# Kernel tuning notes

Measured on AMD Instinct MI355X. Metric: run time of the kernel, lower is better.

Reference implementation:

```python
import jax, jax.numpy as jnp
import numpy as np

P = 6            # number of polynomial moment potentials phi_j(x) = x^j, j=1..P
SIGMA = 0.5      # diffusion coefficient
REG = (1e-3, 0.0, 0.0)  # (scale, threshold, bump) diagonal regularization of G
N_SAMPLES = 2_000_000
N_TIME = 33


def _moments(x):
    # x: (N,1) -> (N,P) with phi_j(x) = x^j (exponents are integral floats, pow is exact)
    js = jnp.arange(1, P + 1, dtype=x.dtype)
    return x ** js


def _grad_pot(x):
    # grad phi_j(x) = j * x^(j-1): (N,1) -> (N,P)
    js = jnp.arange(1, P + 1, dtype=x.dtype)
    return js * x ** (js - 1)


def _G(x):
    # Gram matrix of potential gradients, (P,P), with diagonal regularization
    g = _grad_pot(x)                      # (N,P)
    G = g.T @ g / x.shape[0]
    d = jnp.diag(G)
    d = jnp.where(d < REG[1], d + REG[2], d)
    return G + REG[0] * jnp.diag(d)


def _interp(x_0, x_1, tk):
    # 'Cos' stochastic interpolant I_t = cos(pi t/2) x_0 + sin(pi t/2) x_1
    a = jnp.cos(jnp.pi * tk / 2)
    b = jnp.sin(jnp.pi * tk / 2)
    return a * x_0 + b * x_1


def _dinterp(x_0, x_1, tk):
    c = jnp.pi / 2
    return c * (-jnp.sin(jnp.pi * tk / 2) * x_0 + jnp.cos(jnp.pi * tk / 2) * x_1)


def _rhs_dt(I, Idot):
    # mean_n grad_phi(I)_np * Idot_n  -> (P,)
    return jnp.einsum('np,n->p', _grad_pot(I), Idot[:, 0]) / I.shape[0]


def _sde_forward(x_1, x_0, x_k, t):
    K = t.shape[0]
    key = jax.random.key(42)

    @jax.checkpoint
    def step(x, k):
        tk = t[k]
        tk1 = t[k + 1]
        h = tk1 - tk
        # predictor: eta_k solves G(x_k) eta = E[grad phi(I_k) . dI_k/dt]
        I_k = _interp(x_0, x_1, tk)
        Idot_k = _dinterp(x_0, x_1, tk)
        eta = jnp.linalg.solve(_G(x), _rhs_dt(I_k, Idot_k))       # (P,)
        drift = _grad_pot(x) @ eta                                 # (N,)
        noise = jnp.sqrt(2 * h) * SIGMA * jax.random.normal(
            jax.random.fold_in(key, k), x.shape, x.dtype)
        y = x + h * drift[:, None] + noise
        # corrector: theta_k matches moments of y to the interpolant at t_{k+1}
        I_k1 = _interp(x_0, x_1, tk1)
        bpe = _moments(I_k1).mean(0)                               # (P,)
        rhs_cc = bpe - _moments(y).mean(0)
        theta = jnp.linalg.solve(_G(y), rhs_cc)                    # (P,)
        x_next = y + (_grad_pot(y) @ theta)[:, None]
        theta = theta / (h * SIGMA ** 2)
        dtphi = _rhs_dt(I_k1, Idot_k)   # source uses gradient_interpolant(k) here
        dH = -theta @ dtphi
        bpp = _moments(x_next).mean(0)
        return x_next, (eta, theta, dH, bpe, bpp)

    x_final, (etas, thetas, dHs, bpe_s, bpp_s) = jax.lax.scan(step, x_k, jnp.arange(K - 1))
    # torch code appends the last stored quantities once more after the loop
    barphi_e = jnp.concatenate([_moments(x_0).mean(0)[None], bpe_s, bpe_s[-1:]], 0)
    barphi_p = jnp.concatenate([_moments(x_k).mean(0)[None], bpp_s, bpp_s[-1:]], 0)
    eta_all = jnp.concatenate([etas, etas[-1:]], 0)
    theta_all = jnp.concatenate([thetas, thetas[-1:]], 0)
    dH_all = jnp.concatenate([dHs, dHs[-1:]], 0)
    return x_final, barphi_e, barphi_p, eta_all, theta_all, dH_all


def setup_inputs() -> dict:
    key = jax.random.key(0)
    k1, k2, k3 = jax.random.split(key, 3)
    return {
        'x_1': jax.random.normal(k1, (N_SAMPLES, 1), jnp.float32),
        'x_0': jax.random.normal(k2, (N_SAMPLES, 1), jnp.float32),
        'x_k': jax.random.normal(k3, (N_SAMPLES, 1), jnp.float32),
        't': jnp.linspace(0.0, 1.0, N_TIME, dtype=jnp.float32),
    }


def reference(x_1, x_0, x_k, t):
    return _sde_forward(x_1, x_0, x_k, t)
```

## Files before the change

kernel.cpp:

```cpp
#include <hip/hip_runtime.h>
#include <stdint.h>

#define N_SAMP  2000000
#define NF4     500000
#define NSTEP   32
#define INV_N   (1.0/2000000.0)
#define NBUCK   64
#define GRID    512
#define NWORK   511
#define BLKSZ   256

#define OUT_BE  2000000
#define OUT_BP  2000204
#define OUT_ETA 2000408
#define OUT_TH  2000606
#define OUT_DH  2000804

#define O_JB    0
#define O_SYB   (37*NBUCK)
#define O_SXB   (O_SYB + NSTEP*10*NBUCK)
#define O_END   (O_SXB + NSTEP*10*NBUCK)
#define WS_BYTES (O_END*8 + 1152*4)

#define CFENCE() __atomic_signal_fence(__ATOMIC_SEQ_CST)
#define WAITVM() __builtin_amdgcn_s_waitcnt(0)

__device__ inline uint32_t uld(const uint32_t* p) {
  return __hip_atomic_load(p, __ATOMIC_RELAXED, __HIP_MEMORY_SCOPE_AGENT);
}
__device__ inline void ust(uint32_t* p, uint32_t v) {
  __hip_atomic_store(p, v, __ATOMIC_RELAXED, __HIP_MEMORY_SCOPE_AGENT);
}
__device__ inline void uadd(uint32_t* p, uint32_t v) {
  __hip_atomic_fetch_add(p, v, __ATOMIC_RELAXED, __HIP_MEMORY_SCOPE_AGENT);
}
__device__ inline double dld(const double* p) {
  return __hip_atomic_load(p, __ATOMIC_RELAXED, __HIP_MEMORY_SCOPE_AGENT);
}
__device__ inline float fld(const float* p) {
  return __hip_atomic_load(p, __ATOMIC_RELAXED, __HIP_MEMORY_SCOPE_AGENT);
}
__device__ inline void fst(float* p, float v) {
  __hip_atomic_store(p, v, __ATOMIC_RELAXED, __HIP_MEMORY_SCOPE_AGENT);
}

__host__ __device__ inline void threefry2x32(uint32_t k0, uint32_t k1,
                                             uint32_t c0, uint32_t c1,
                                             uint32_t* o0, uint32_t* o1) {
  uint32_t ks2 = k0 ^ k1 ^ 0x1BD11BDAu;
  uint32_t x0 = c0 + k0;
  uint32_t x1 = c1 + k1;
#define TF_ROT(x, d) (((x) << (d)) | ((x) >> (32 - (d))))
#define TF_R(a,b,c,d, ka, kb, inc) \
  x0 += x1; x1 = TF_ROT(x1, a); x1 ^= x0; \
  x0 += x1; x1 = TF_ROT(x1, b); x1 ^= x0; \
  x0 += x1; x1 = TF_ROT(x1, c); x1 ^= x0; \
  x0 += x1; x1 = TF_ROT(x1, d); x1 ^= x0; \
  x0 += (ka); x1 += (kb) + (inc);
  TF_R(13,15,26,6,  k1,  ks2, 1u)
  TF_R(17,29,16,24, ks2, k0,  2u)
  TF_R(13,15,26,6,  k0,  k1,  3u)
  TF_R(17,29,16,24, k1,  ks2, 4u)
  TF_R(13,15,26,6,  ks2, k0,  5u)
#undef TF_R
#undef TF_ROT
  *o0 = x0; *o1 = x1;
}

__device__ inline float bits_to_normal(uint32_t bits) {
  float f = __uint_as_float((bits >> 9) | 0x3f800000u) - 1.0f;
  const float lo = -0.99999994f;
  float u = f * 2.0f + lo;
  u = fmaxf(lo, u);
  float w = -log1pf(-u * u);
  float p;
  if (w < 5.0f) {
    w = w - 2.5f;
    p = 2.81022636e-08f;
    p = fmaf(p, w, 3.43273939e-07f);
    p = fmaf(p, w, -3.5233877e-06f);
    p = fmaf(p, w, -4.39150654e-06f);
    p = fmaf(p, w, 0.00021858087f);
    p = fmaf(p, w, -0.00125372503f);
    p = fmaf(p, w, -0.00417768164f);
    p = fmaf(p, w, 0.246640727f);
    p = fmaf(p, w, 1.50140941f);
  } else {
    w = sqrtf(w) - 3.0f;
    p = -0.000200214257f;
    p = fmaf(p, w, 0.000100950558f);
    p = fmaf(p, w, 0.00134934322f);
    p = fmaf(p, w, -0.00367342844f);
    p = fmaf(p, w, 0.00573950773f);
    p = fmaf(p, w, -0.0076224613f);
    p = fmaf(p, w, 0.00943887047f);
    p = fmaf(p, w, 1.00167406f);
    p = fmaf(p, w, 2.83297682f);
  }
  return __uint_as_float(0x3FB504F3u) * (p * u);
}

__device__ inline double wave_gauss6(const double S[11], double rv, int lane) {
  int r = (lane < 6) ? lane : 0;
  double row[6];
#pragma unroll
  for (int j = 0; j < 6; j++) row[j] = (double)((r + 1) * (j + 1)) * S[r + j];
  row[r] *= 1.001;
#pragma unroll
  for (int c = 0; c < 6; c++) {
    double pr[6], prh;
#pragma unroll
    for (int j = 0; j < 6; j++) pr[j] = __shfl(row[j], c, 64);
    prh = __shfl(rv, c, 64);
    if (lane > c && lane < 6) {
      double f = row[c] / pr[c];
#pragma unroll
      for (int j = 0; j < 6; j++) row[j] -= f * pr[j];
      rv -= f * prh;
    }
  }
  double xv = 0.0;
#pragma unroll
  for (int rr = 5; rr >= 0; rr--) {
    double cand = rv / row[rr];
    double xr = __shfl(cand, rr, 64);
    if (lane == rr) xv = xr;
    if (lane < rr) rv -= row[rr] * xr;
  }
  return xv;
}

__device__ inline void wait_leaves(const uint32_t* leaf, uint32_t target, int lane) {
  for (;;) {
    uint32_t v = uld(&leaf[lane & 31]);
#pragma unroll
    for (int off = 16; off; off >>= 1) v += __shfl_xor(v, off, 64);
    if (v >= target) break;
    __builtin_amdgcn_s_sleep(2);
  }
  CFENCE();
}

__device__ inline void get_S(const double* B, int lane, double S[11]) {
  S[0] = 1.0;
#pragma unroll
  for (int q = 0; q < 10; q++) {
    double s = dld(&B[q * NBUCK + lane]);
#pragma unroll
    for (int off = 32; off; off >>= 1) s += __shfl_xor(s, off, 64);
    S[q + 1] = s * INV_N;
  }
}

template <int NQ>
__device__ inline void block_bucket(float acc[NQ], double* __restrict__ buck,
                                    float smf[4][37], int lane, int wid, int t,
                                    int bidx) {
#pragma unroll
  for (int q = 0; q < NQ; q++) {
    float v = acc[q];
#pragma unroll
    for (int off = 32; off; off >>= 1) v += __shfl_down(v, off, 64);
    if (lane == 0) smf[wid][q] = v;
  }
  __syncthreads();
  if (t < NQ) {
    double s = (double)smf[0][t] + (double)smf[1][t] +
               (double)smf[2][t] + (double)smf[3][t];
    atomicAdd(&buck[t * NBUCK + bidx], s);
  }
}

__global__ __launch_bounds__(BLKSZ, 2) void k_all(
    const float* __restrict__ x1g, const float* __restrict__ x0g,
    const float* __restrict__ xkg, const float* __restrict__ tg,
    float* __restrict__ out, double* __restrict__ WD, uint32_t* __restrict__ WU) {
  __shared__ float smf[4][37];
  __shared__ float sC[8];
  __shared__ double sMsc[37];
  __shared__ float sF[NSTEP * 20];
  __shared__ uint32_t sK[NSTEP][2];

  const int t = threadIdx.x;
  const int lane = t & 63, wid = t >> 6;
  double* JB  = WD + O_JB;
  double* SYB = WD + O_SYB;
  double* SXB = WD + O_SXB;
  float* COEFP = (float*)WU;
  float* COEFC = (float*)(WU + 8);
  uint32_t* leaf0 = WU + 32;
  uint32_t* leafP = WU + 64;
  uint32_t* leafC = WU + 96;
  uint32_t* seqP  = WU + 128;
  uint32_t* seqC  = WU + 640;

  if (blockIdx.x == 0) {
    if (t >= 64) return;
    wait_leaves(leaf0, NWORK, lane);
    for (int q = 0; q < 37; q++) {
      double s = dld(&JB[q * NBUCK + lane]);
#pragma unroll
      for (int off = 32; off; off >>= 1) s += __shfl_xor(s, off, 64);
      if (lane == 0) sMsc[q] = s * INV_N;
    }
#define MG(A, B_) (((A) == 0 && (B_) == 0) ? 1.0 : \
    sMsc[(((A) + (B_) + 2) * ((A) + (B_) - 1)) / 2 + (A)])
    if (lane < NSTEP) {
      const double Bd[7][7] = {
          {1,0,0,0,0,0,0},{1,1,0,0,0,0,0},{1,2,1,0,0,0,0},{1,3,3,1,0,0,0},
          {1,4,6,4,1,0,0},{1,5,10,10,5,1,0},{1,6,15,20,15,6,1}};
      int k = lane;
      float tk = tg[k], tk1 = tg[k + 1];
      float h = tk1 - tk;
      float ns = sqrtf(2.0f * h) * 0.5f;
      const float PI_F = 3.14159274f;
      double a  = (double)cosf((PI_F * tk) * 0.5f);
      double b  = (double)sinf((PI_F * tk) * 0.5f);
      double a1 = (double)cosf((PI_F * tk1) * 0.5f);
      double b1 = (double)sinf((PI_F * tk1) * 0.5f);
      const double C2 = (double)1.57079637f;
      double pa[7], pb[7], pa1[7], pb1[7];
      pa[0] = pb[0] = pa1[0] = pb1[0] = 1.0;
      for (int i = 1; i < 7; i++) {
        pa[i] = pa[i-1] * a;   pb[i] = pb[i-1] * b;
        pa1[i] = pa1[i-1] * a1; pb1[i] = pb1[i-1] * b1;
      }
      sF[k * 20 + 0] = h;
      sF[k * 20 + 1] = ns;
      for (int p = 1; p <= 6; p++) {
        double s_rhs = 0, s_bpe = 0, s_dt = 0;
        for (int j = 0; j < p; j++) {
          double term = -b * MG(j + 1, p - 1 - j) + a * MG(j, p - j);
          s_rhs += Bd[p-1][j] * pa[j]  * pb[p-1-j]  * term;
          s_dt  += Bd[p-1][j] * pa1[j] * pb1[p-1-j] * term;
        }
        for (int j = 0; j <= p; j++)
          s_bpe += Bd[p][j] * pa1[j] * pb1[p - j] * MG(j, p - j);
        float fr = (float)((double)p * C2 * s_rhs);
        float be = (float)s_bpe;
        sF[k * 20 + 2 + p - 1]  = fr;
        sF[k * 20 + 8 + p - 1]  = be;
        sF[k * 20 + 14 + p - 1] = (float)((double)p * C2 * s_dt);
        out[OUT_BE + (k + 1) * 6 + (p - 1)] = be;
        if (k == NSTEP - 1) out[OUT_BE + (NSTEP + 1) * 6 + (p - 1)] = be;
      }
    }
    if (lane < 6) {
      int p = lane + 1;
      out[OUT_BE + lane] = (float)MG(p, 0);
      out[OUT_BP + lane] = (float)sMsc[27 + lane];
    }
#undef MG
    {
      double S[11];
      S[0] = 1.0;
#pragma unroll
      for (int q = 0; q < 10; q++) S[q + 1] = sMsc[27 + q];
      double rv = (lane < 6) ? (double)sF[2 + lane] : 0.0;
      double xv = wave_gauss6(S, rv, lane);
      if (lane < 6) {
        out[OUT_ETA + lane] = (float)xv;
        fst(&COEFP[lane], (float)xv * (float)(lane + 1));
      }
      if (lane == 6) fst(&COEFP[6], sF[0]);
      if (lane == 7) fst(&COEFP[7], sF[1]);
      CFENCE(); WAITVM();
      if (lane < 32) ust(&seqP[lane * 16], 1u);
    }
    for (int k = 0; k < NSTEP; k++) {
      wait_leaves(leafP, (uint32_t)(NWORK * (k + 1)), lane);
      {
        double S[11];
        get_S(SYB + k * 10 * NBUCK, lane, S);
        double rv = (lane < 6) ? ((double)sF[k*20 + 8 + lane] - S[lane + 1]) : 0.0;
        double xv = wave_gauss6(S, rv, lane);
        if (lane < 6) fst(&COEFC[lane], (float)xv * (float)(lane + 1));
        float h = sF[k * 20];
        float th = (float)xv / (h * 0.25f);
        if (lane < 6) {
          out[OUT_TH + k * 6 + lane] = th;
          if (k == NSTEP - 1) out[OUT_TH + NSTEP * 6 + lane] = th;
        }
        float contrib = (lane < 6) ? th * sF[k*20 + 14 + lane] : 0.f;
#pragma unroll
        for (int off = 4; off; off >>= 1) contrib += __shfl_down(contrib, off, 64);
        if (lane == 0) {
          float dH = -contrib;
          out[OUT_DH + k] = dH;
          if (k == NSTEP - 1) out[OUT_DH + NSTEP] = dH;
        }
        CFENCE(); WAITVM();
        if (lane < 32) ust(&seqC[lane * 16], (uint32_t)(k + 1));
      }
      wait_leaves(leafC, (uint32_t)(NWORK * (k + 1)), lane);
      {
        double S[11];
        get_S(SXB + k * 10 * NBUCK, lane, S);
        if (lane < 6) {
          float bp = (float)S[lane + 1];
          out[OUT_BP + (k + 1) * 6 + lane] = bp;
          if (k == NSTEP - 1) out[OUT_BP + (NSTEP + 1) * 6 + lane] = bp;
        }
        if (k < NSTEP - 1) {
          double rv = (lane < 6) ? (double)sF[(k+1)*20 + 2 + lane] : 0.0;
          double xv = wave_gauss6(S, rv, lane);
          if (lane < 6) {
            float v = (float)xv;
            out[OUT_ETA + (k + 1) * 6 + lane] = v;
            if (k + 1 == NSTEP - 1) out[OUT_ETA + NSTEP * 6 + lane] = v;
            fst(&COEFP[lane], v * (float)(lane + 1));
          }
          if (lane == 6) fst(&COEFP[6], sF[(k+1) * 20 + 0]);
          if (lane == 7) fst(&COEFP[7], sF[(k+1) * 20 + 1]);
          CFENCE(); WAITVM();
          if (lane < 32) ust(&seqP[lane * 16], (uint32_t)(k + 2));
        }
      }
    }
    return;
  }

  const int wb = blockIdx.x - 1;
  const int bidx = blockIdx.x & (NBUCK - 1);
  const int myseq = (blockIdx.x & 31) * 16;
  int f4[4]; bool vld[4];
  float st[16];
  float nz[16];
  if (t < NSTEP) threefry2x32(0u, 42u, 0u, (uint32_t)t, &sK[t][0], &sK[t][1]);
#pragma unroll
  for (int c = 0; c < 4; c++) { f4[c] = (wb * 4 + c) * 256 + t; vld[c] = f4[c] < NF4; }

  {
    float a37[37];
#pragma unroll
    for (int q = 0; q < 37; q++) a37[q] = 0.f;
#pragma unroll
    for (int c = 0; c < 4; c++) {
      if (vld[c]) {
        float4 xk4 = ((const float4*)xkg)[f4[c]];
        float4 x04 = ((const float4*)x0g)[f4[c]];
        float4 x14 = ((const float4*)x1g)[f4[c]];
        float xk_[4] = {xk4.x, xk4.y, xk4.z, xk4.w};
        float x0_[4] = {x04.x, x04.y, x04.z, x04.w};
        float x1_[4] = {x14.x, x14.y, x14.z, x14.w};
#pragma unroll
        for (int r = 0; r < 4; r++) {
          st[c * 4 + r] = xk_[r];
          float p0[7], p1[7];
          p0[0] = 1.f; p1[0] = 1.f;
#pragma unroll
          for (int m = 0; m < 6; m++) { p0[m+1] = p0[m]*x0_[r]; p1[m+1] = p1[m]*x1_[r]; }
          int q = 0;
#pragma unroll
          for (int s = 1; s <= 6; s++)
#pragma unroll
            for (int a = 0; a <= s; a++) a37[q++] += p0[a] * p1[s - a];
          float xp = xk_[r];
          a37[27] += xp;
#pragma unroll
          for (int m = 1; m < 10; m++) { xp *= xk_[r]; a37[27 + m] += xp; }
        }
      } else {
#pragma unroll
        for (int r = 0; r < 4; r++) st[c * 4 + r] = 0.f;
      }
    }
    block_bucket<37>(a37, JB, smf, lane, wid, t, bidx);
    if (t == 0) { CFENCE(); WAITVM(); uadd(&leaf0[blockIdx.x & 31], 1u); }
  }

#pragma unroll
  for (int c = 0; c < 4; c++) {
    if (vld[c]) {
      uint32_t base = (uint32_t)(f4[c] * 4);
#pragma unroll
      for (int r = 0; r < 4; r++) {
        uint32_t o0, o1;
        threefry2x32(sK[0][0], sK[0][1], 0u, base + (uint32_t)r, &o0, &o1);
        nz[c * 4 + r] = bits_to_normal(o0 ^ o1);
      }
    }
  }

  for (int k = 0; k < NSTEP; k++) {
    if (t == 0) {
      while (uld(&seqP[myseq]) < (uint32_t)(k + 1)) __builtin_amdgcn_s_sleep(2);
      CFENCE();
#pragma unroll
      for (int i = 0; i < 8; i++) sC[i] = fld(&COEFP[i]);
    }
    __syncthreads();
    {
      float c0 = sC[0], c1 = sC[1], c2 = sC[2], c3 = sC[3];
      float c4 = sC[4], c5 = sC[5], h = sC[6], ns = sC[7];
      float acc[10];
#pragma unroll
      for (int q = 0; q < 10; q++) acc[q] = 0.f;
#pragma unroll
      for (int c = 0; c < 4; c++) {
        if (vld[c]) {
#pragma unroll
          for (int r = 0; r < 4; r++) {
            float x = st[c * 4 + r];
            float d = c0 + x*(c1 + x*(c2 + x*(c3 + x*(c4 + x*c5))));
            float y = x + h * d + ns * nz[c * 4 + r];
            st[c * 4 + r] = y;
            float pw = y;
            acc[0] += pw;
#pragma unroll
            for (int m = 1; m < 10; m++) { pw *= y; acc[m] += pw; }
          }
        }
      }
      block_bucket<10>(acc, SYB + k * 10 * NBUCK, smf, lane, wid, t, bidx);
      if (t == 0) { CFENCE(); WAITVM(); uadd(&leafP[blockIdx.x & 31], 1u); }
    }
    if (k + 1 < NSTEP) {
      uint32_t ka = sK[k + 1][0], kb = sK[k + 1][1];
#pragma unroll
      for (int c = 0; c < 4; c++) {
        if (vld[c]) {
          uint32_t base = (uint32_t)(f4[c] * 4);
#pragma unroll
          for (int r = 0; r < 4; r++) {
            uint32_t o0, o1;
            threefry2x32(ka, kb, 0u, base + (uint32_t)r, &o0, &o1);
            nz[c * 4 + r] = bits_to_normal(o0 ^ o1);
          }
        }
      }
    }
    if (t == 0) {
      while (uld(&seqC[myseq]) < (uint32_t)(k + 1)) __builtin_amdgcn_s_sleep(2);
      CFENCE();
#pragma unroll
      for (int i = 0; i < 6; i++) sC[i] = fld(&COEFC[i]);
    }
    __syncthreads();
    {
      float c0 = sC[0], c1 = sC[1], c2 = sC[2], c3 = sC[3];
      float c4 = sC[4], c5 = sC[5];
      float acc[10];
#pragma unroll
      for (int q = 0; q < 10; q++) acc[q] = 0.f;
#pragma unroll
      for (int c = 0; c < 4; c++) {
        if (vld[c]) {
#pragma unroll
          for (int r = 0; r < 4; r++) {
            float y = st[c * 4 + r];
            float cr = c0 + y*(c1 + y*(c2 + y*(c3 + y*(c4 + y*c5))));
            float xn = y + cr;
            st[c * 4 + r] = xn;
            float pw = xn;
            acc[0] += pw;
#pragma unroll
            for (int m = 1; m < 10; m++) { pw *= xn; acc[m] += pw; }
          }
        }
      }
      block_bucket<10>(acc, SXB + k * 10 * NBUCK, smf, lane, wid, t, bidx);
      if (t == 0) { CFENCE(); WAITVM(); uadd(&leafC[blockIdx.x & 31], 1u); }
    }
  }

#pragma unroll
  for (int c = 0; c < 4; c++) {
    if (vld[c]) {
      ((float4*)out)[f4[c]] =
          make_float4(st[c*4+0], st[c*4+1], st[c*4+2], st[c*4+3]);
    }
  }
}

extern "C" void kernel_launch(void* const* d_in, const int* in_sizes, int n_in,
                              void* d_out, int out_size, void* d_ws, size_t ws_size,
                              hipStream_t stream) {
  const float* x1 = (const float*)d_in[0];
  const float* x0 = (const float*)d_in[1];
  const float* xk = (const float*)d_in[2];
  const float* t  = (const float*)d_in[3];
  float* out = (float*)d_out;

  double* WD = (double*)d_ws;
  uint32_t* WU = (uint32_t*)(WD + O_END);

  hipMemsetAsync(d_ws, 0, (size_t)WS_BYTES, stream);
  k_all<<<GRID, BLKSZ, 0, stream>>>(x1, x0, xk, t, out, WD, WU);
}
```

Before: 873.6 us.

## Replace sequence flags with tagged 64-bit coefficient words and split RNG work

Each coefficient is now packed with its step tag into one 64-bit atomic word and replicated 8 times, so worker blocks poll the coefficients directly. This removes the separate sequence-flag store and its fence/waitcnt round trip on the coordinator. The coordinator publishes the next predictor coefficients before writing the bp outputs, shortening the critical path. Half of the next-step threefry noise generation moves to after the corrector phase, to spread compute across both waits. The moment powers now use a shallower multiply tree. The cost is wider polling reads on the worker side.

```diff
diff --git a/kernel.cpp b/kernel.cpp
--- a/kernel.cpp
+++ b/kernel.cpp
@@ -20,7 +20,7 @@
 #define O_SYB   (37*NBUCK)
 #define O_SXB   (O_SYB + NSTEP*10*NBUCK)
 #define O_END   (O_SXB + NSTEP*10*NBUCK)
-#define WS_BYTES (O_END*8 + 1152*4)
+#define WS_BYTES (O_END*8 + 128*4 + 128*8)
 
 #define CFENCE() __atomic_signal_fence(__ATOMIC_SEQ_CST)
 #define WAITVM() __builtin_amdgcn_s_waitcnt(0)
@@ -28,19 +28,16 @@
 __device__ inline uint32_t uld(const uint32_t* p) {
   return __hip_atomic_load(p, __ATOMIC_RELAXED, __HIP_MEMORY_SCOPE_AGENT);
 }
-__device__ inline void ust(uint32_t* p, uint32_t v) {
-  __hip_atomic_store(p, v, __ATOMIC_RELAXED, __HIP_MEMORY_SCOPE_AGENT);
-}
 __device__ inline void uadd(uint32_t* p, uint32_t v) {
   __hip_atomic_fetch_add(p, v, __ATOMIC_RELAXED, __HIP_MEMORY_SCOPE_AGENT);
 }
 __device__ inline double dld(const double* p) {
   return __hip_atomic_load(p, __ATOMIC_RELAXED, __HIP_MEMORY_SCOPE_AGENT);
 }
-__device__ inline float fld(const float* p) {
+__device__ inline unsigned long long ald64(const unsigned long long* p) {
   return __hip_atomic_load(p, __ATOMIC_RELAXED, __HIP_MEMORY_SCOPE_AGENT);
 }
-__device__ inline void fst(float* p, float v) {
+__device__ inline void ast64(unsigned long long* p, unsigned long long v) {
   __hip_atomic_store(p, v, __ATOMIC_RELAXED, __HIP_MEMORY_SCOPE_AGENT);
 }
 
@@ -152,6 +149,14 @@
   }
 }
 
+__device__ inline void publish8(unsigned long long* base, int lane,
+                                uint32_t tag, float val) {
+  int i = lane & 7, rep = lane >> 3;
+  unsigned long long w =
+      ((unsigned long long)tag << 32) | (unsigned long long)__float_as_uint(val);
+  ast64(&base[(size_t)rep * 8 + i], w);
+}
+
 template <int NQ>
 __device__ inline void block_bucket(float acc[NQ], double* __restrict__ buck,
                                     float smf[4][37], int lane, int wid, int t,
@@ -169,6 +174,36 @@
                (double)smf[2][t] + (double)smf[3][t];
     atomicAdd(&buck[t * NBUCK + bidx], s);
   }
+}
+
+__device__ inline void poll_coefs(const unsigned long long* cp, uint32_t want,
+                                  float* sC, int t) {
+  if (t == 0) {
+    for (;;) {
+      unsigned long long w[8];
+#pragma unroll
+      for (int i = 0; i < 8; i++) w[i] = ald64(&cp[i]);
+      bool ok = true;
+#pragma unroll
+      for (int i = 0; i < 8; i++) ok = ok && ((uint32_t)(w[i] >> 32) == want);
+      if (ok) {
+#pragma unroll
+        for (int i = 0; i < 8; i++) sC[i] = __uint_as_float((uint32_t)w[i]);
+        break;
+      }
+      __builtin_amdgcn_s_sleep(2);
+    }
+  }
+  __syncthreads();
+}
+
+__device__ inline void acc_moments(float y, float acc[10]) {
+  float p2 = y * y;
+  float p3 = p2 * y, p4 = p2 * p2;
+  float p5 = p3 * p2, p6 = p3 * p3, p7 = p4 * p3, p8 = p4 * p4;
+  float p9 = p5 * p4, p10 = p5 * p5;
+  acc[0] += y;  acc[1] += p2; acc[2] += p3; acc[3] += p4; acc[4] += p5;
+  acc[5] += p6; acc[6] += p7; acc[7] += p8; acc[8] += p9; acc[9] += p10;
 }
 
 __global__ __launch_bounds__(BLKSZ, 2) void k_all(
@@ -186,13 +221,12 @@
   double* JB  = WD + O_JB;
   double* SYB = WD + O_SYB;
   double* SXB = WD + O_SXB;
-  float* COEFP = (float*)WU;
-  float* COEFC = (float*)(WU + 8);
   uint32_t* leaf0 = WU + 32;
   uint32_t* leafP = WU + 64;
   uint32_t* leafC = WU + 96;
-  uint32_t* seqP  = WU + 128;
-  uint32_t* seqC  = WU + 640;
+  unsigned long long* C64  = (unsigned long long*)(WU + 128);
+  unsigned long long* C64P = C64;
+  unsigned long long* C64C = C64 + 64;
 
   if (blockIdx.x == 0) {
     if (t >= 64) return;
@@ -245,28 +279,25 @@
         if (k == NSTEP - 1) out[OUT_BE + (NSTEP + 1) * 6 + (p - 1)] = be;
       }
     }
+    {
+      double S[11];
+      S[0] = 1.0;
+#pragma unroll
+      for (int q = 0; q < 10; q++) S[q + 1] = sMsc[27 + q];
+      double rv = (lane < 6) ? (double)sF[2 + lane] : 0.0;
+      double xv = wave_gauss6(S, rv, lane);
+      int i = lane & 7;
+      float xs = (float)__shfl(xv, i, 64);
+      float val = (i < 6) ? xs * (float)(i + 1) : ((i == 6) ? sF[0] : sF[1]);
+      publish8(C64P, lane, 1u, val);
+      if (lane < 6) out[OUT_ETA + lane] = (float)xv;
+    }
     if (lane < 6) {
       int p = lane + 1;
       out[OUT_BE + lane] = (float)MG(p, 0);
       out[OUT_BP + lane] = (float)sMsc[27 + lane];
     }
 #undef MG
-    {
-      double S[11];
-      S[0] = 1.0;
-#pragma unroll
-      for (int q = 0; q < 10; q++) S[q + 1] = sMsc[27 + q];
-      double rv = (lane < 6) ? (double)sF[2 + lane] : 0.0;
-      double xv = wave_gauss6(S, rv, lane);
-      if (lane < 6) {
-        out[OUT_ETA + lane] = (float)xv;
-        fst(&COEFP[lane], (float)xv * (float)(lane + 1));
-      }
-      if (lane == 6) fst(&COEFP[6], sF[0]);
-      if (lane == 7) fst(&COEFP[7], sF[1]);
-      CFENCE(); WAITVM();
-      if (lane < 32) ust(&seqP[lane * 16], 1u);
-    }
     for (int k = 0; k < NSTEP; k++) {
       wait_leaves(leafP, (uint32_t)(NWORK * (k + 1)), lane);
       {
@@ -274,7 +305,10 @@
         get_S(SYB + k * 10 * NBUCK, lane, S);
         double rv = (lane < 6) ? ((double)sF[k*20 + 8 + lane] - S[lane + 1]) : 0.0;
         double xv = wave_gauss6(S, rv, lane);
-        if (lane < 6) fst(&COEFC[lane], (float)xv * (float)(lane + 1));
+        int i = lane & 7;
+        float xs = (float)__shfl(xv, i, 64);
+        float val = (i < 6) ? xs * (float)(i + 1) : 0.f;
+        publish8(C64C, lane, (uint32_t)(k + 1), val);
         float h = sF[k * 20];
         float th = (float)xv / (h * 0.25f);
         if (lane < 6) {
@@ -289,32 +323,30 @@
           out[OUT_DH + k] = dH;
           if (k == NSTEP - 1) out[OUT_DH + NSTEP] = dH;
         }
-        CFENCE(); WAITVM();
-        if (lane < 32) ust(&seqC[lane * 16], (uint32_t)(k + 1));
       }
       wait_leaves(leafC, (uint32_t)(NWORK * (k + 1)), lane);
       {
         double S[11];
         get_S(SXB + k * 10 * NBUCK, lane, S);
+        if (k < NSTEP - 1) {
+          double rv = (lane < 6) ? (double)sF[(k+1)*20 + 2 + lane] : 0.0;
+          double xv = wave_gauss6(S, rv, lane);
+          int i = lane & 7;
+          float xs = (float)__shfl(xv, i, 64);
+          float val = (i < 6) ? xs * (float)(i + 1)
+                              : ((i == 6) ? sF[(k+1)*20 + 0] : sF[(k+1)*20 + 1]);
+          publish8(C64P, lane, (uint32_t)(k + 2), val);
+          if (lane < 6) {
+            float v = (float)xv;
+            out[OUT_ETA + (k + 1) * 6 + lane] = v;
+            if (k + 1 == NSTEP - 1) out[OUT_ETA + NSTEP * 6 + lane] = v;
+          }
+        }
         if (lane < 6) {
           float bp = (float)S[lane + 1];
           out[OUT_BP + (k + 1) * 6 + lane] = bp;
           if (k == NSTEP - 1) out[OUT_BP + (NSTEP + 1) * 6 + lane] = bp;
         }
-        if (k < NSTEP - 1) {
-          double rv = (lane < 6) ? (double)sF[(k+1)*20 + 2 + lane] : 0.0;
-          double xv = wave_gauss6(S, rv, lane);
-          if (lane < 6) {
-            float v = (float)xv;
-            out[OUT_ETA + (k + 1) * 6 + lane] = v;
-            if (k + 1 == NSTEP - 1) out[OUT_ETA + NSTEP * 6 + lane] = v;
-            fst(&COEFP[lane], v * (float)(lane + 1));
-          }
-          if (lane == 6) fst(&COEFP[6], sF[(k+1) * 20 + 0]);
-          if (lane == 7) fst(&COEFP[7], sF[(k+1) * 20 + 1]);
-          CFENCE(); WAITVM();
-          if (lane < 32) ust(&seqP[lane * 16], (uint32_t)(k + 2));
-        }
       }
     }
     return;
@@ -322,7 +354,8 @@
 
   const int wb = blockIdx.x - 1;
   const int bidx = blockIdx.x & (NBUCK - 1);
-  const int myseq = (blockIdx.x & 31) * 16;
+  const unsigned long long* myP = C64P + (size_t)(blockIdx.x & 7) * 8;
+  const unsigned long long* myC = C64C + (size_t)(blockIdx.x & 7) * 8;
   int f4[4]; bool vld[4];
   float st[16];
   float nz[16];
@@ -383,13 +416,7 @@
   }
 
   for (int k = 0; k < NSTEP; k++) {
-    if (t == 0) {
-      while (uld(&seqP[myseq]) < (uint32_t)(k + 1)) __builtin_amdgcn_s_sleep(2);
-      CFENCE();
-#pragma unroll
-      for (int i = 0; i < 8; i++) sC[i] = fld(&COEFP[i]);
-    }
-    __syncthreads();
+    poll_coefs(myP, (uint32_t)(k + 1), sC, t);
     {
       float c0 = sC[0], c1 = sC[1], c2 = sC[2], c3 = sC[3];
       float c4 = sC[4], c5 = sC[5], h = sC[6], ns = sC[7];
@@ -405,10 +432,7 @@
             float d = c0 + x*(c1 + x*(c2 + x*(c3 + x*(c4 + x*c5))));
             float y = x + h * d + ns * nz[c * 4 + r];
             st[c * 4 + r] = y;
-            float pw = y;
-            acc[0] += pw;
-#pragma unroll
-            for (int m = 1; m < 10; m++) { pw *= y; acc[m] += pw; }
+            acc_moments(y, acc);
           }
         }
       }
@@ -418,7 +442,7 @@
     if (k + 1 < NSTEP) {
       uint32_t ka = sK[k + 1][0], kb = sK[k + 1][1];
 #pragma unroll
-      for (int c = 0; c < 4; c++) {
+      for (int c = 0; c < 2; c++) {
         if (vld[c]) {
           uint32_t base = (uint32_t)(f4[c] * 4);
 #pragma unroll
@@ -430,13 +454,7 @@
         }
       }
     }
-    if (t == 0) {
-      while (uld(&seqC[myseq]) < (uint32_t)(k + 1)) __builtin_amdgcn_s_sleep(2);
-      CFENCE();
-#pragma unroll
-      for (int i = 0; i < 6; i++) sC[i] = fld(&COEFC[i]);
-    }
-    __syncthreads();
+    poll_coefs(myC, (uint32_t)(k + 1), sC, t);
     {
       float c0 = sC[0], c1 = sC[1], c2 = sC[2], c3 = sC[3];
       float c4 = sC[4], c5 = sC[5];
@@ -452,15 +470,27 @@
             float cr = c0 + y*(c1 + y*(c2 + y*(c3 + y*(c4 + y*c5))));
             float xn = y + cr;
             st[c * 4 + r] = xn;
-            float pw = xn;
-            acc[0] += pw;
-#pragma unroll
-            for (int m = 1; m < 10; m++) { pw *= xn; acc[m] += pw; }
+            acc_moments(xn, acc);
           }
         }
       }
       block_bucket<10>(acc, SXB + k * 10 * NBUCK, smf, lane, wid, t, bidx);
       if (t == 0) { CFENCE(); WAITVM(); uadd(&leafC[blockIdx.x & 31], 1u); }
+    }
+    if (k + 1 < NSTEP) {
+      uint32_t ka = sK[k + 1][0], kb = sK[k + 1][1];
+#pragma unroll
+      for (int c = 2; c < 4; c++) {
+        if (vld[c]) {
+          uint32_t base = (uint32_t)(f4[c] * 4);
+#pragma unroll
+          for (int r = 0; r < 4; r++) {
+            uint32_t o0, o1;
+            threefry2x32(ka, kb, 0u, base + (uint32_t)r, &o0, &o1);
+            nz[c * 4 + r] = bits_to_normal(o0 ^ o1);
+          }
+        }
+      }
     }
   }
 
```

After: 730.8 us. -16.4%, faster.
